# Performance work log

Hardware: AMD Instinct MI355X
Metric: run time of the kernel (lower is better)

Reference implementation:

```python
import jax, jax.numpy as jnp
import numpy as np

N = 100000
E = 1600000
D_IN, D_OUT = 25, 50


def _seg_softmax(scores, seg, num_segments):
    m = jax.ops.segment_max(scores, seg, num_segments=num_segments)
    e = jnp.exp(scores - m[seg])
    s = jax.ops.segment_sum(e, seg, num_segments=num_segments)
    return e / (s[seg] + 1e-16)


def gatv2_conv(x, ei, Wl, bl, Wr, br, att, bo):
    # PyG GATv2Conv, heads=1, concat=True, add_self_loops=True, negative_slope=0.2
    n = x.shape[0]
    loops = jnp.arange(n, dtype=ei.dtype)
    src = jnp.concatenate([ei[0], loops])  # message sources j
    dst = jnp.concatenate([ei[1], loops])  # message targets i
    xl = x @ Wl + bl  # [N, 50] source transform
    xr = x @ Wr + br  # [N, 50] target transform
    m = jax.nn.leaky_relu(xl[src] + xr[dst], 0.2)  # [E+N, 50]
    scores = m @ att  # [E+N]
    alpha = _seg_softmax(scores, dst, n)
    out = jax.ops.segment_sum(alpha[:, None] * xl[src], dst, num_segments=n)
    return out + bo


def setup_inputs() -> dict:
    key = jax.random.key(0)
    ks = jax.random.split(key, 32)
    d = {}
    d['x'] = jax.random.normal(ks[0], (N, D_IN), dtype=jnp.float32)
    d['ei_p'] = jax.random.randint(ks[1], (2, E), 0, N, dtype=jnp.int32)
    d['ei_s'] = jax.random.randint(ks[2], (2, E), 0, N, dtype=jnp.int32)
    d['ei_v'] = jax.random.randint(ks[3], (2, E), 0, N, dtype=jnp.int32)
    i = 4
    for tag in ('p', 's', 'v'):
        d['Wl_' + tag] = jax.random.normal(ks[i], (D_IN, D_OUT), dtype=jnp.float32) * 0.2; i += 1
        d['bl_' + tag] = jnp.zeros((D_OUT,), jnp.float32)
        d['Wr_' + tag] = jax.random.normal(ks[i], (D_IN, D_OUT), dtype=jnp.float32) * 0.2; i += 1
        d['br_' + tag] = jnp.zeros((D_OUT,), jnp.float32)
        d['att_' + tag] = jax.random.normal(ks[i], (D_OUT,), dtype=jnp.float32) * 0.2; i += 1
        d['bo_' + tag] = jnp.zeros((D_OUT,), jnp.float32)
    d['proj_W'] = jax.random.normal(ks[i], (150, 150), dtype=jnp.float32) * 0.08; i += 1
    d['proj_b'] = jnp.zeros((150,), jnp.float32)
    d['cls_W1'] = jax.random.normal(ks[i], (150, 75), dtype=jnp.float32) * 0.08; i += 1
    d['cls_b1'] = jnp.zeros((75,), jnp.float32)
    d['cls_W2'] = jax.random.normal(ks[i], (75, 30), dtype=jnp.float32) * 0.12; i += 1
    d['cls_b2'] = jnp.zeros((30,), jnp.float32)
    d['cls_W3'] = jax.random.normal(ks[i], (30, 2), dtype=jnp.float32) * 0.18; i += 1
    d['cls_b3'] = jnp.zeros((2,), jnp.float32)
    return d


def reference(x, ei_p, ei_s, ei_v,
              Wl_p, bl_p, Wr_p, br_p, att_p, bo_p,
              Wl_s, bl_s, Wr_s, br_s, att_s, bo_s,
              Wl_v, bl_v, Wr_v, br_v, att_v, bo_v,
              proj_W, proj_b, cls_W1, cls_b1, cls_W2, cls_b2, cls_W3, cls_b3):
    act = lambda h: jax.nn.leaky_relu(h, 0.1)
    x_p = act(gatv2_conv(x, ei_p, Wl_p, bl_p, Wr_p, br_p, att_p, bo_p))
    x_s = act(gatv2_conv(x, ei_s, Wl_s, bl_s, Wr_s, br_s, att_s, bo_s))
    x_v = act(gatv2_conv(x, ei_v, Wl_v, bl_v, Wr_v, br_v, att_v, bo_v))
    h = jnp.concatenate((x_p, x_s, x_v), axis=1)  # [N, 150]
    h = h @ proj_W + proj_b
    h = act(h @ cls_W1 + cls_b1)
    h = act(h @ cls_W2 + cls_b2)
    return h @ cls_W3 + cls_b3  # [N, 2]
```

## Files before the change

kernel.cpp:

```cpp
#include <hip/hip_runtime.h>
#include <hip/hip_fp16.h>

#define N_NODES 100000
#define N_EDGES 1600000
#define D_IN 25
#define D_OUT 50
#define NBKT 391
#define EPB 8192
#define NBLK_E 196
#define BSTR 4736
#define CAP 5888

typedef __attribute__((ext_vector_type(8))) _Float16 half8;
typedef __attribute__((ext_vector_type(2))) _Float16 h2;
typedef __attribute__((ext_vector_type(4))) float float4v;

__device__ __forceinline__ float lrelu(float x, float a) { return fmaxf(x, a * x); }
__device__ __forceinline__ h2 bch2(unsigned u) { return __builtin_bit_cast(h2, u); }

__global__ __launch_bounds__(256) void bkt_scatter_kernel(
    const int* __restrict__ eip, const int* __restrict__ eis, const int* __restrict__ eiv,
    unsigned* __restrict__ bcur3, unsigned* __restrict__ bucketed3)
{
    int t = blockIdx.y;
    const int* ei = (t == 0) ? eip : ((t == 1) ? eis : eiv);
    unsigned* bcur = bcur3 + t * NBKT;
    unsigned* bucketed = bucketed3 + (size_t)t * NBKT * BSTR;
    __shared__ unsigned h[NBKT];
    __shared__ unsigned cur[NBKT];
    int tid = threadIdx.x;
    for (int b = tid; b < NBKT; b += 256) h[b] = 0;
    __syncthreads();
#pragma unroll
    for (int i = 0; i < EPB / 256; ++i) {
        int e = blockIdx.x * EPB + i * 256 + tid;
        if (e < N_EDGES) atomicAdd(&h[ei[N_EDGES + e] >> 8], 1u);
    }
    __syncthreads();
    for (int b = tid; b < NBKT; b += 256)
        cur[b] = (unsigned)b * BSTR + (h[b] ? atomicAdd(&bcur[b], h[b]) : 0u);
    __syncthreads();
#pragma unroll
    for (int i = 0; i < EPB / 256; ++i) {
        int e = blockIdx.x * EPB + i * 256 + tid;
        if (e < N_EDGES) {
            unsigned s = (unsigned)ei[e];
            unsigned d = (unsigned)ei[N_EDGES + e];
            unsigned b = d >> 8;
            unsigned r = atomicAdd(&cur[b], 1u);
            if (r < (b + 1u) * BSTR)
                bucketed[r] = ((d & 255u) << 17) | s;
        }
    }
}

__device__ __forceinline__ void pack_seg(
    const float* __restrict__ W, unsigned short* __restrict__ outp,
    int K, int O, int NKS, int idx)
{
    int f = idx >> 9, r = idx & 511;
    int l = r >> 3, j = r & 7;
    int ot = f / NKS, ks = f - ot * NKS;
    int k = ks * 32 + (l >> 4) * 8 + j;
    int o = ot * 16 + (l & 15);
    float val = (k < K && o < O) ? W[k * O + o] : 0.f;
    outp[idx] = __half_as_ushort(__float2half_rn(val));
}

__global__ __launch_bounds__(256) void pack_all_kernel(
    const float* __restrict__ projW, const float* __restrict__ W1,
    const float* __restrict__ W2, const float* __restrict__ W3,
    const float* __restrict__ b0, const float* __restrict__ b1,
    const float* __restrict__ b2, const float* __restrict__ b3,
    const float* __restrict__ Wl0, const float* __restrict__ Wr0,
    const float* __restrict__ Wl1, const float* __restrict__ Wr1,
    const float* __restrict__ Wl2, const float* __restrict__ Wr2,
    const float* __restrict__ bl0, const float* __restrict__ br0,
    const float* __restrict__ bl1, const float* __restrict__ br1,
    const float* __restrict__ bl2, const float* __restrict__ br2,
    unsigned short* __restrict__ wpkAll, float* __restrict__ biasPad,
    __half* __restrict__ xl3)
{
    int gid = blockIdx.x * 256 + threadIdx.x;
    if (gid < 25600) pack_seg(projW, wpkAll, 150, 150, 5, gid);
    else if (gid < 40960) pack_seg(W1, wpkAll + 25600, 150, 75, 5, gid - 25600);
    else if (gid < 44032) pack_seg(W2, wpkAll + 40960, 75, 30, 3, gid - 40960);
    else if (gid < 44544) pack_seg(W3, wpkAll + 44032, 30, 2, 1, gid - 44032);
    else if (gid < 56832) {
        int t = gid - 44544;
        int mat = t >> 11, idx = t & 2047;
        const float* Wm = (mat == 0) ? Wl0 : (mat == 1) ? Wr0 : (mat == 2) ? Wl1
                        : (mat == 3) ? Wr1 : (mat == 4) ? Wl2 : Wr2;
        int ot = idx >> 9, r = idx & 511;
        int l = r >> 3, j = r & 7;
        int k = (l >> 4) * 8 + j;
        int o = ot * 16 + (l & 15);
        float val = (k < D_IN && o < D_OUT) ? Wm[k * D_OUT + o] : 0.f;
        wpkAll[44544 + t] = __half_as_ushort(__float2half_rn(val));
    } else if (gid < 57520) {
        int t = gid - 56832;
        float v;
        if (t < 304) {
            if (t < 160) v = (t < 150) ? b0[t] : 0.f;
            else if (t < 256) { int i = t - 160; v = (i < 75) ? b1[i] : 0.f; }
            else if (t < 288) { int i = t - 256; v = (i < 30) ? b2[i] : 0.f; }
            else { int i = t - 288; v = (i < 2) ? b3[i] : 0.f; }
        } else {
            int ii = t - 304;
            int mat = ii >> 6, o = ii & 63;
            const float* bm = (mat == 0) ? bl0 : (mat == 1) ? br0 : (mat == 2) ? bl1
                            : (mat == 3) ? br1 : (mat == 4) ? bl2 : br2;
            v = (o < D_OUT) ? bm[o] : 0.f;
        }
        biasPad[t] = v;
    } else if (gid < 57584) {
        xl3[(size_t)3 * N_NODES * 64 + (gid - 57520)] = __ushort_as_half((unsigned short)0);
    }
}

#define TSTR 32
#define OSTR 72

__global__ __launch_bounds__(256) void transform_mfma_kernel(
    const float* __restrict__ x,
    const unsigned short* __restrict__ wpkAll, const float* __restrict__ biasPad,
    __half* __restrict__ xl3, __half* __restrict__ xr3)
{
    __shared__ _Float16 sX[64 * TSTR];
    __shared__ _Float16 sO[4][16 * OSTR];
    int tid = threadIdx.x;
    int w = tid >> 6, l = tid & 63;
    int g0 = blockIdx.x * 64;
    for (int i = tid; i < 64 * D_IN; i += 256) {
        int r = i / D_IN, c = i - r * D_IN;
        int gr = g0 + r;
        sX[r * TSTR + c] = (gr < N_NODES) ? (_Float16)x[(size_t)gr * D_IN + c] : (_Float16)0.f;
    }
    for (int i = tid; i < 64 * 7; i += 256) {
        int r = i / 7, c = D_IN + (i - r * 7);
        sX[r * TSTR + c] = (_Float16)0.f;
    }
    __syncthreads();
    int lm = l & 15, q = l >> 4;
    half8 a = *(const half8*)(sX + (w * 16 + lm) * TSTR + q * 8);
    const unsigned short* wT = wpkAll + 44544;
#pragma unroll
    for (int mat = 0; mat < 6; ++mat) {
        float4v acc[4];
#pragma unroll
        for (int ot = 0; ot < 4; ++ot) {
            half8 b = *(const half8*)(wT + (mat * 4 + ot) * 512 + l * 8);
            float4v z = {0.f, 0.f, 0.f, 0.f};
            acc[ot] = __builtin_amdgcn_mfma_f32_16x16x32_f16(a, b, z, 0, 0, 0);
        }
#pragma unroll
        for (int ot = 0; ot < 4; ++ot) {
            float bv = biasPad[304 + mat * 64 + ot * 16 + lm];
#pragma unroll
            for (int r = 0; r < 4; ++r)
                sO[w][(q * 4 + r) * OSTR + ot * 16 + lm] = (_Float16)(acc[ot][r] + bv);
        }
        __half* dst = ((mat & 1) ? xr3 : xl3) + (size_t)(mat >> 1) * N_NODES * 64;
#pragma unroll
        for (int it = 0; it < 2; ++it) {
            int idx = it * 64 + l;
            int rr = idx >> 3, cc = idx & 7;
            int gr = g0 + w * 16 + rr;
            if (gr < N_NODES) {
                uint4 v = *(const uint4*)&sO[w][rr * OSTR + cc * 8];
                *(uint4*)&dst[(size_t)gr * 64 + cc * 8] = v;
            }
        }
    }
}

__device__ __forceinline__ float edge_score8(uint4 u, const h2* xr, const h2* at)
{
    const h2 k2 = {(_Float16)0.2f, (_Float16)0.2f};
    float acc = 0.f;
    unsigned uu[4] = {u.x, u.y, u.z, u.w};
#pragma unroll
    for (int i = 0; i < 4; ++i) {
        h2 m = bch2(uu[i]) + xr[i];
        m = __builtin_elementwise_max(m, m * k2);
        acc = __builtin_amdgcn_fdot2(m, at[i], acc, false);
    }
    return acc;
}
__device__ __forceinline__ void accum8(float2* O, float w, uint4 u)
{
    unsigned uu[4] = {u.x, u.y, u.z, u.w};
#pragma unroll
    for (int i = 0; i < 4; ++i) {
        h2 xv = bch2(uu[i]);
        O[i].x += w * (float)xv[0];
        O[i].y += w * (float)xv[1];
    }
}

__global__ __launch_bounds__(256) void bkt_gat_kernel(
    const unsigned* __restrict__ bucketed3, const unsigned* __restrict__ bcur3,
    const __half* __restrict__ xl3, const __half* __restrict__ xr3,
    const float* __restrict__ att0, const float* __restrict__ att1, const float* __restrict__ att2,
    const float* __restrict__ bo0, const float* __restrict__ bo1, const float* __restrict__ bo2,
    __half* __restrict__ h16)
{
    int tag = blockIdx.y, b = blockIdx.x;
    const unsigned* bucketed = bucketed3 + (size_t)tag * NBKT * BSTR + (size_t)b * BSTR;
    const uint4* xl4 = (const uint4*)xl3 + (size_t)tag * N_NODES * 8;
    const uint4* xr4 = (const uint4*)xr3 + (size_t)tag * N_NODES * 8;
    const float* att = (tag == 0) ? att0 : (tag == 1) ? att1 : att2;
    const float* bo  = (tag == 0) ? bo0  : (tag == 1) ? bo1  : bo2;
    int col0 = tag * 50;

    __shared__ unsigned hist[256];
    __shared__ unsigned dstart[257];
    __shared__ unsigned cur[256];
    __shared__ unsigned srcsL[CAP];
    int tid = threadIdx.x;
    unsigned cnt = bcur3[tag * NBKT + b];
    if (cnt > BSTR) cnt = BSTR;
    hist[tid] = 0;
    __syncthreads();
    for (unsigned i = tid; i < cnt; i += 256) atomicAdd(&hist[bucketed[i] >> 17], 1u);
    __syncthreads();
    unsigned c = hist[tid];
    unsigned pc = (c + 3u) & ~3u;
    hist[tid] = pc;
    __syncthreads();
    for (int off = 1; off < 256; off <<= 1) {
        unsigned v = (tid >= off) ? hist[tid - off] : 0;
        __syncthreads();
        hist[tid] += v;
        __syncthreads();
    }
    unsigned excl = hist[tid] - pc;
    dstart[tid] = excl;
    cur[tid] = excl;
    if (tid == 255) dstart[256] = hist[255];
    __syncthreads();
    for (unsigned i = tid; i < cnt; i += 256) {
        unsigned w = bucketed[i];
        unsigned r = atomicAdd(&cur[w >> 17], 1u);
        srcsL[r] = (w & 0x1FFFFu) << 3;
    }
    const unsigned DUMMY = 0x80000000u | ((unsigned)((3 - tag) * N_NODES) << 3);
    for (unsigned k = c; k < pc; ++k) srcsL[excl + k] = DUMMY;
    __syncthreads();

    const int l = tid & 7, grp = tid >> 3;
    int c0 = 8 * l;
    h2 at[4];
#pragma unroll
    for (int i = 0; i < 4; ++i) {
        int cc = c0 + 2 * i;
        float lo = (cc < D_OUT) ? att[cc] : 0.f;
        float hi = (cc + 1 < D_OUT) ? att[cc + 1] : 0.f;
        at[i] = h2{(_Float16)lo, (_Float16)hi};
    }
    for (int d8 = 0; d8 < 8; ++d8) {
        int d = grp * 8 + d8;
        int g = (b << 8) + d;
        if (g >= N_NODES) break;
        uint4 xru = xr4[g * 8 + l];
        h2 xr[4] = {bch2(xru.x), bch2(xru.y), bch2(xru.z), bch2(xru.w)};
        uint4 xs = xl4[g * 8 + l];

        float q = edge_score8(xs, xr, at);
        q += __shfl_xor(q, 1); q += __shfl_xor(q, 2); q += __shfl_xor(q, 4);
        float S = __expf(q);
        float2 O[4] = {{0.f, 0.f}, {0.f, 0.f}, {0.f, 0.f}, {0.f, 0.f}};
        accum8(O, S, xs);

        unsigned j = dstart[d], jE = dstart[d + 1];
        if (j < jE) {
            uint4 vv = *(const uint4*)&srcsL[j];
            uint4 c0v = xl4[(vv.x & 0x7FFFFFFFu) + l];
            uint4 c1v = xl4[(vv.y & 0x7FFFFFFFu) + l];
            uint4 c2v = xl4[(vv.z & 0x7FFFFFFFu) + l];
            uint4 c3v = xl4[(vv.w & 0x7FFFFFFFu) + l];
            for (;;) {
                j += 4;
                bool more = j < jE;
                uint4 nv, p0v, p1v, p2v, p3v;
                if (more) {
                    nv = *(const uint4*)&srcsL[j];
                    p0v = xl4[(nv.x & 0x7FFFFFFFu) + l];
                    p1v = xl4[(nv.y & 0x7FFFFFFFu) + l];
                    p2v = xl4[(nv.z & 0x7FFFFFFFu) + l];
                    p3v = xl4[(nv.w & 0x7FFFFFFFu) + l];
                }
                float p0 = edge_score8(c0v, xr, at);
                float p1 = edge_score8(c1v, xr, at);
                float p2 = edge_score8(c2v, xr, at);
                float p3 = edge_score8(c3v, xr, at);
                p0 += __shfl_xor(p0, 1); p0 += __shfl_xor(p0, 2); p0 += __shfl_xor(p0, 4);
                p1 += __shfl_xor(p1, 1); p1 += __shfl_xor(p1, 2); p1 += __shfl_xor(p1, 4);
                p2 += __shfl_xor(p2, 1); p2 += __shfl_xor(p2, 2); p2 += __shfl_xor(p2, 4);
                p3 += __shfl_xor(p3, 1); p3 += __shfl_xor(p3, 2); p3 += __shfl_xor(p3, 4);
                float w0 = (vv.x & 0x80000000u) ? 0.f : __expf(p0);
                float w1 = (vv.y & 0x80000000u) ? 0.f : __expf(p1);
                float w2 = (vv.z & 0x80000000u) ? 0.f : __expf(p2);
                float w3 = (vv.w & 0x80000000u) ? 0.f : __expf(p3);
                S += (w0 + w1) + (w2 + w3);
                accum8(O, w0, c0v);
                accum8(O, w1, c1v);
                accum8(O, w2, c2v);
                accum8(O, w3, c3v);
                if (!more) break;
                vv = nv; c0v = p0v; c1v = p1v; c2v = p2v; c3v = p3v;
            }
        }
        float inv = 1.f / (S + 1e-16f);
        size_t base = (size_t)g * 160 + col0 + c0;
#pragma unroll
        for (int i = 0; i < 4; ++i) {
            int cc = c0 + 2 * i;
            if (cc + 1 < D_OUT) {
                float blo = bo[cc], bhi = bo[cc + 1];
                float vlo = lrelu(O[i].x * inv + blo, 0.1f);
                float vhi = lrelu(O[i].y * inv + bhi, 0.1f);
                *(__half2*)&h16[base + 2 * i] = __floats2half2_rn(vlo, vhi);
            }
        }
    }
}

#define HS 168

template<int NOT, int NKS, bool ACT>
__device__ __forceinline__ void head_layer(
    const _Float16* __restrict__ in, _Float16* __restrict__ outp,
    const unsigned short* __restrict__ wp, const float* __restrict__ bias, int l)
{
    const int lm = l & 15, q = l >> 4;
    const _Float16* aBase = in + lm * HS + q * 8;
#pragma unroll
    for (int ot = 0; ot < NOT; ++ot) {
        float4v acc = {0.f, 0.f, 0.f, 0.f};
        const unsigned short* bBase = wp + (ot * NKS) * 512 + l * 8;
#pragma unroll
        for (int ks = 0; ks < NKS; ++ks) {
            half8 a = *(const half8*)(aBase + ks * 32);
            half8 b = *(const half8*)(bBase + ks * 512);
            acc = __builtin_amdgcn_mfma_f32_16x16x32_f16(a, b, acc, 0, 0, 0);
        }
        float bv = bias[ot * 16 + lm];
#pragma unroll
        for (int r = 0; r < 4; ++r) {
            float v = acc[r] + bv;
            if (ACT) v = lrelu(v, 0.1f);
            outp[(q * 4 + r) * HS + ot * 16 + lm] = (_Float16)v;
        }
    }
}

__global__ __launch_bounds__(256) void mfma_head_kernel(
    const __half* __restrict__ h16,
    const unsigned short* __restrict__ wpkAll, const float* __restrict__ biasPad,
    float* __restrict__ out)
{
    __shared__ _Float16 sIn[4][16 * HS];
    __shared__ _Float16 sOut[4][16 * HS];
    int tid = threadIdx.x;
    int w = tid >> 6, l = tid & 63;
    int g0 = blockIdx.x * 64 + w * 16;

    const uint2* hq = (const uint2*)h16;
    for (int idx = l; idx < 16 * 42; idx += 64) {
        int row = idx / 42, qc = idx - row * 42;
        int gn = g0 + row;
        uint2 u = {0u, 0u};
        if (gn < N_NODES && qc < 40) {
            u = hq[(size_t)gn * 40 + qc];
            if (qc == 37) u.y = 0u;
            else if (qc > 37) { u.x = 0u; u.y = 0u; }
        }
        *(uint2*)&sIn[w][row * HS + qc * 4] = u;
    }
    __syncthreads();
    head_layer<10, 5, false>(sIn[w], sOut[w], wpkAll,         biasPad + 0,   l);
    __syncthreads();
    head_layer<6, 5, true >(sOut[w], sIn[w], wpkAll + 25600,  biasPad + 160, l);
    __syncthreads();
    head_layer<2, 3, true >(sIn[w], sOut[w], wpkAll + 40960,  biasPad + 256, l);
    __syncthreads();
    {
        const int lm = l & 15, q = l >> 4;
        float4v acc = {0.f, 0.f, 0.f, 0.f};
        half8 a = *(const half8*)(sOut[w] + lm * HS + q * 8);
        half8 b = *(const half8*)(wpkAll + 44032 + l * 8);
        acc = __builtin_amdgcn_mfma_f32_16x16x32_f16(a, b, acc, 0, 0, 0);
        if (lm < 2) {
            float bv = biasPad[288 + lm];
#pragma unroll
            for (int r = 0; r < 4; ++r) {
                int node = g0 + q * 4 + r;
                if (node < N_NODES) out[node * 2 + lm] = acc[r] + bv;
            }
        }
    }
}

extern "C" void kernel_launch(void* const* d_in, const int* in_sizes, int n_in,
                              void* d_out, int out_size, void* d_ws, size_t ws_size,
                              hipStream_t stream)
{
    const float* x = (const float*)d_in[0];
    const int* eip = (const int*)d_in[1];
    const int* eis = (const int*)d_in[2];
    const int* eiv = (const int*)d_in[3];
    const float *Wl[3], *bl[3], *Wr[3], *br[3], *att[3], *bo[3];
    for (int t = 0; t < 3; ++t) {
        int b = 4 + t * 6;
        Wl[t] = (const float*)d_in[b + 0];
        bl[t] = (const float*)d_in[b + 1];
        Wr[t] = (const float*)d_in[b + 2];
        br[t] = (const float*)d_in[b + 3];
        att[t] = (const float*)d_in[b + 4];
        bo[t] = (const float*)d_in[b + 5];
    }
    const float* projW = (const float*)d_in[22];
    const float* projb = (const float*)d_in[23];
    const float* W1 = (const float*)d_in[24];
    const float* b1 = (const float*)d_in[25];
    const float* W2 = (const float*)d_in[26];
    const float* b2 = (const float*)d_in[27];
    const float* W3 = (const float*)d_in[28];
    const float* b3 = (const float*)d_in[29];
    float* out = (float*)d_out;

    char* ws = (char*)d_ws;
    size_t off = 0;
    auto alloc = [&](size_t bytes) -> char* {
        char* p = ws + off;
        off += (bytes + 255) & ~(size_t)255;
        return p;
    };
    __half* xl3 = (__half*)alloc(((size_t)3 * N_NODES * 64 + 64) * 2);
    __half* xr3 = (__half*)alloc((size_t)3 * N_NODES * 64 * 2);
    unsigned* bucketed3 = (unsigned*)alloc((size_t)3 * NBKT * BSTR * 4);
    unsigned* bcur3 = (unsigned*)alloc((size_t)3 * NBKT * 4);
    __half* h16 = (__half*)alloc((size_t)N_NODES * 160 * 2);
    unsigned short* wpkAll = (unsigned short*)alloc(56832 * 2);
    float* biasPad = (float*)alloc(688 * 4);

    hipMemsetAsync(bcur3, 0, (size_t)3 * NBKT * 4, stream);
    pack_all_kernel<<<226, 256, 0, stream>>>(
        projW, W1, W2, W3, projb, b1, b2, b3,
        Wl[0], Wr[0], Wl[1], Wr[1], Wl[2], Wr[2],
        bl[0], br[0], bl[1], br[1], bl[2], br[2],
        wpkAll, biasPad, xl3);

    bkt_scatter_kernel<<<dim3(NBLK_E, 3), 256, 0, stream>>>(eip, eis, eiv, bcur3, bucketed3);

    transform_mfma_kernel<<<(N_NODES + 63) / 64, 256, 0, stream>>>(
        x, wpkAll, biasPad, xl3, xr3);

    bkt_gat_kernel<<<dim3(NBKT, 3), 256, 0, stream>>>(
        bucketed3, bcur3, xl3, xr3,
        att[0], att[1], att[2], bo[0], bo[1], bo[2], h16);

    mfma_head_kernel<<<(N_NODES + 63) / 64, 256, 0, stream>>>(h16, wpkAll, biasPad, out);
}
```

Measured before the change: 406.1 us.

## Halve bucket size and dynamically assign destination nodes to lane groups

Destination buckets shrink from 256 to 128 nodes, doubling the number of aggregation blocks and cutting the per-block shared staging buffer. Inside each block, every 8-lane group now fetches its next destination node from a shared atomic counter instead of owning a fixed eight nodes. This targets load imbalance from uneven in-degrees and is meant to raise occupancy. In exchange it adds per-node shared atomics and shuffles, and the bucket scatter kernel needs more bucket counters. The padding dummy index is also changed to a fixed offset.

```diff
diff --git a/kernel.cpp b/kernel.cpp
--- a/kernel.cpp
+++ b/kernel.cpp
@@ -5,11 +5,11 @@
 #define N_EDGES 1600000
 #define D_IN 25
 #define D_OUT 50
-#define NBKT 391
+#define NBKT 782
 #define EPB 8192
 #define NBLK_E 196
-#define BSTR 4736
-#define CAP 5888
+#define BSTR 2560
+#define CAP 2944
 
 typedef __attribute__((ext_vector_type(8))) _Float16 half8;
 typedef __attribute__((ext_vector_type(2))) _Float16 h2;
@@ -34,7 +34,7 @@
 #pragma unroll
     for (int i = 0; i < EPB / 256; ++i) {
         int e = blockIdx.x * EPB + i * 256 + tid;
-        if (e < N_EDGES) atomicAdd(&h[ei[N_EDGES + e] >> 8], 1u);
+        if (e < N_EDGES) atomicAdd(&h[ei[N_EDGES + e] >> 7], 1u);
     }
     __syncthreads();
     for (int b = tid; b < NBKT; b += 256)
@@ -46,10 +46,10 @@
         if (e < N_EDGES) {
             unsigned s = (unsigned)ei[e];
             unsigned d = (unsigned)ei[N_EDGES + e];
-            unsigned b = d >> 8;
+            unsigned b = d >> 7;
             unsigned r = atomicAdd(&cur[b], 1u);
             if (r < (b + 1u) * BSTR)
-                bucketed[r] = ((d & 255u) << 17) | s;
+                bucketed[r] = ((d & 127u) << 17) | s;
         }
     }
 }
@@ -213,42 +213,53 @@
     const float* bo  = (tag == 0) ? bo0  : (tag == 1) ? bo1  : bo2;
     int col0 = tag * 50;
 
-    __shared__ unsigned hist[256];
-    __shared__ unsigned dstart[257];
-    __shared__ unsigned cur[256];
+    __shared__ unsigned hist[128];
+    __shared__ unsigned dstart[129];
+    __shared__ unsigned cur[128];
     __shared__ unsigned srcsL[CAP];
+    __shared__ unsigned nextD;
     int tid = threadIdx.x;
     unsigned cnt = bcur3[tag * NBKT + b];
     if (cnt > BSTR) cnt = BSTR;
-    hist[tid] = 0;
+    if (tid < 128) hist[tid] = 0;
+    if (tid == 0) nextD = 0;
     __syncthreads();
     for (unsigned i = tid; i < cnt; i += 256) atomicAdd(&hist[bucketed[i] >> 17], 1u);
     __syncthreads();
-    unsigned c = hist[tid];
-    unsigned pc = (c + 3u) & ~3u;
-    hist[tid] = pc;
-    __syncthreads();
-    for (int off = 1; off < 256; off <<= 1) {
-        unsigned v = (tid >= off) ? hist[tid - off] : 0;
+    unsigned c = 0, pc = 0;
+    if (tid < 128) {
+        c = hist[tid];
+        pc = (c + 3u) & ~3u;
+        hist[tid] = pc;
+    }
+    __syncthreads();
+    for (int off = 1; off < 128; off <<= 1) {
+        unsigned v = (tid >= off && tid < 128) ? hist[tid - off] : 0;
         __syncthreads();
-        hist[tid] += v;
+        if (tid < 128) hist[tid] += v;
         __syncthreads();
     }
-    unsigned excl = hist[tid] - pc;
-    dstart[tid] = excl;
-    cur[tid] = excl;
-    if (tid == 255) dstart[256] = hist[255];
+    if (tid < 128) {
+        unsigned excl = hist[tid] - pc;
+        dstart[tid] = excl;
+        cur[tid] = excl;
+        if (tid == 127) dstart[128] = hist[127];
+    }
     __syncthreads();
     for (unsigned i = tid; i < cnt; i += 256) {
         unsigned w = bucketed[i];
         unsigned r = atomicAdd(&cur[w >> 17], 1u);
         srcsL[r] = (w & 0x1FFFFu) << 3;
     }
-    const unsigned DUMMY = 0x80000000u | ((unsigned)((3 - tag) * N_NODES) << 3);
-    for (unsigned k = c; k < pc; ++k) srcsL[excl + k] = DUMMY;
-    __syncthreads();
-
-    const int l = tid & 7, grp = tid >> 3;
+    if (tid < 128) {
+        const unsigned DUMMY = 0x80000000u | ((unsigned)(3 * N_NODES) << 3);
+        unsigned excl = dstart[tid];
+        for (unsigned k = c; k < pc; ++k) srcsL[excl + k] = DUMMY;
+    }
+    __syncthreads();
+
+    const int l = tid & 7;
+    const int grpBase = tid & ~7;
     int c0 = 8 * l;
     h2 at[4];
 #pragma unroll
@@ -258,10 +269,13 @@
         float hi = (cc + 1 < D_OUT) ? att[cc + 1] : 0.f;
         at[i] = h2{(_Float16)lo, (_Float16)hi};
     }
-    for (int d8 = 0; d8 < 8; ++d8) {
-        int d = grp * 8 + d8;
-        int g = (b << 8) + d;
-        if (g >= N_NODES) break;
+    for (;;) {
+        unsigned d;
+        if (l == 0) d = atomicAdd(&nextD, 1u);
+        d = (unsigned)__shfl((int)d, grpBase);
+        if (d >= 128u) break;
+        int g = (b << 7) + (int)d;
+        if (g >= N_NODES) continue;
         uint4 xru = xr4[g * 8 + l];
         h2 xr[4] = {bch2(xru.x), bch2(xru.y), bch2(xru.z), bch2(xru.w)};
         uint4 xs = xl4[g * 8 + l];
```

Measured after the change: 390.0 us. 4.0% less time.
